# Kernel optimization log

Measured on AMD Instinct MI355X. Metric: run time of the kernel, lower is better.

The kernel has to match this reference:

```python
import jax, jax.numpy as jnp
import numpy as np

DIM = 1024
NUM_ATT = 8
NUM_HEADS = 16
HEAD_DIM = DIM // NUM_HEADS
ROPE_BASE = 10000.0
NEG_INF = -1e9


def _rope(x):
    # x: [B, H, L, hd]; torchtune-style interleaved RoPE applied along the sequence axis.
    B, H, L, hd = x.shape
    pos = jnp.arange(L, dtype=jnp.float32)
    inv_freq = 1.0 / (ROPE_BASE ** (jnp.arange(0, hd, 2, dtype=jnp.float32) / hd))
    ang = pos[:, None] * inv_freq[None, :]          # [L, hd/2]
    cos = jnp.cos(ang)[None, None]                  # [1,1,L,hd/2]
    sin = jnp.sin(ang)[None, None]
    xr = x.reshape(B, H, L, hd // 2, 2)
    x0, x1 = xr[..., 0], xr[..., 1]
    out = jnp.stack([x0 * cos - x1 * sin, x1 * cos + x0 * sin], axis=-1)
    return out.reshape(B, H, L, hd).astype(x.dtype)


def setup_inputs() -> dict:
    key = jax.random.key(0)
    ks = jax.random.split(key, 7)
    B, L = 32, 512
    x = jax.random.normal(ks[0], (B, L, DIM), dtype=jnp.float32)
    s = 0.02  # init scale for numerical sanity (init choice, not math)
    query_projs = jax.random.normal(ks[1], (NUM_ATT, DIM, DIM), dtype=jnp.float32) * s
    key_projs = jax.random.normal(ks[2], (NUM_ATT, DIM, DIM), dtype=jnp.float32) * s
    value_projs = jax.random.normal(ks[3], (NUM_ATT, DIM, DIM), dtype=jnp.float32) * s
    out_projs = jax.random.normal(ks[4], (NUM_ATT, DIM, DIM), dtype=jnp.float32) * s
    router_w = jax.random.normal(ks[5], (DIM, NUM_ATT), dtype=jnp.float32) * s
    router_b = jnp.zeros((NUM_ATT,), dtype=jnp.float32)
    return {"x": x, "query_projs": query_projs, "key_projs": key_projs,
            "value_projs": value_projs, "out_projs": out_projs,
            "router_w": router_w, "router_b": router_b}


def reference(x, query_projs, key_projs, value_projs, out_projs, router_w, router_b):
    B, L, D = x.shape
    H, hd = NUM_HEADS, HEAD_DIM
    scale = hd ** -0.5

    # top-1 routing on mean-pooled tokens
    logits = x.mean(axis=1) @ router_w + router_b       # [B, E]
    attn_probs = jax.nn.softmax(logits, axis=-1)
    routes = jnp.argmax(attn_probs, axis=-1)            # [B] int

    # per-batch weight gather (the memory-bound irregular access) + bmm
    qw = query_projs[routes]                             # [B, D, D]
    kw = key_projs[routes]
    vw = value_projs[routes]
    q = jnp.einsum('bld,bde->ble', x, qw)
    k = jnp.einsum('bld,bde->ble', x, kw)
    v = jnp.einsum('bld,bde->ble', x, vw)

    q = q.reshape(B, L, H, hd).transpose(0, 2, 1, 3)     # [B,H,L,hd]
    k = k.reshape(B, L, H, hd).transpose(0, 2, 1, 3)
    v = v.reshape(B, L, H, hd).transpose(0, 2, 1, 3)

    q = _rope(q)
    k = _rope(k)

    scores = jnp.einsum('bhld,bhmd->bhlm', q, k) * scale  # [B,H,L,L]
    causal = jnp.triu(jnp.ones((L, L), dtype=bool), k=1)  # True above diag = masked
    scores = jnp.where(causal[None, None], NEG_INF, scores)
    attn = jax.nn.softmax(scores, axis=-1)
    out = jnp.einsum('bhlm,bhmd->bhld', attn, v)          # [B,H,L,hd]
    out = out.transpose(0, 2, 1, 3).reshape(B, L, D)

    ow = out_projs[routes]                                # [B, D, D]
    out = jnp.einsum('bld,bde->ble', out, ow)
    return out, attn_probs
```

## Files before the change

### kernel.cpp

```cpp
#include <hip/hip_runtime.h>


typedef __attribute__((ext_vector_type(8))) short bf16x8;
typedef __attribute__((ext_vector_type(4))) float f32x4;
typedef __attribute__((ext_vector_type(8))) unsigned short u16x8;

typedef const __attribute__((address_space(1))) unsigned short* gas_t;
typedef __attribute__((address_space(3))) unsigned short* las_t;

#define OFF_PART   (0ull)
#define OFF_ROUTES (2ull << 20)
#define OFF_XB     (3ull << 20)
#define OFF_WT     (40ull << 20)
#define OFF_QKV    (112ull << 20)

__device__ __forceinline__ unsigned short f2bf(float f){
  unsigned int u = __float_as_uint(f);
  u += 0x7fffu + ((u >> 16) & 1u);
  return (unsigned short)(u >> 16);
}
__device__ __forceinline__ float bfu(unsigned int lo16){
  return __uint_as_float(lo16 << 16);
}


__global__ void meanpool_kernel(const float* __restrict__ x, float* __restrict__ part){
  const int b = blockIdx.x, lc = blockIdx.y, t = threadIdx.x;
  const float* xb = x + ((size_t)b*512 + lc*32)*1024;
  float a0=0.f, a1=0.f, a2=0.f, a3=0.f;
  for (int l = 0; l < 32; ++l){
    const float* row = xb + l*1024;
    a0 += row[t]; a1 += row[t+256]; a2 += row[t+512]; a3 += row[t+768];
  }
  float* o = part + ((size_t)b*16 + lc)*1024;
  o[t] = a0; o[t+256] = a1; o[t+512] = a2; o[t+768] = a3;
}

__global__ void router_kernel(const float* __restrict__ part,
                              const float* __restrict__ rw,
                              const float* __restrict__ rbias,
                              float* __restrict__ probs,
                              int* __restrict__ routes){
  const int b = blockIdx.x, t = threadIdx.x;
  __shared__ float xbar[1024];
  __shared__ float red[256*8];
  #pragma unroll
  for (int k = 0; k < 4; ++k){
    const int d = t + k*256;
    float s = 0.f;
    for (int lc = 0; lc < 16; ++lc) s += part[((size_t)b*16 + lc)*1024 + d];
    xbar[d] = s * (1.0f/512.0f);
  }
  __syncthreads();
  float p[8] = {0.f,0.f,0.f,0.f,0.f,0.f,0.f,0.f};
  #pragma unroll
  for (int k = 0; k < 4; ++k){
    const int d = t + k*256;
    const float xv = xbar[d];
    #pragma unroll
    for (int e = 0; e < 8; ++e) p[e] = fmaf(xv, rw[d*8 + e], p[e]);
  }
  #pragma unroll
  for (int e = 0; e < 8; ++e) red[t*8 + e] = p[e];
  __syncthreads();
  for (int s2 = 128; s2 > 0; s2 >>= 1){
    if (t < s2){
      #pragma unroll
      for (int e = 0; e < 8; ++e) red[t*8 + e] += red[(t + s2)*8 + e];
    }
    __syncthreads();
  }
  if (t == 0){
    float lg[8], mx = -3e38f; int am = 0;
    #pragma unroll
    for (int e = 0; e < 8; ++e){
      lg[e] = red[e] + rbias[e];
      if (lg[e] > mx){ mx = lg[e]; am = e; }
    }
    float sum = 0.f, ex[8];
    #pragma unroll
    for (int e = 0; e < 8; ++e){ ex[e] = __expf(lg[e] - mx); sum += ex[e]; }
    const float inv = 1.0f / sum;
    #pragma unroll
    for (int e = 0; e < 8; ++e) probs[b*8 + e] = ex[e] * inv;
    routes[b] = am;
  }
}


__global__ void xcast_kernel(const float4* __restrict__ x, unsigned short* __restrict__ xb){
  const size_t i = (size_t)blockIdx.x * blockDim.x + threadIdx.x;
  const float4 v = x[i];
  ushort4 o;
  o.x = f2bf(v.x); o.y = f2bf(v.y); o.z = f2bf(v.z); o.w = f2bf(v.w);
  *(ushort4*)(xb + 4*i) = o;
}

__global__ void wcast_kernel(const float* __restrict__ W, unsigned short* __restrict__ Wt){
  __shared__ float tile[32][33];
  const int mtx = blockIdx.z;
  const float* Wm = W + (size_t)mtx*1024*1024;
  unsigned short* Wo = Wt + (size_t)mtx*1024*1024;
  const int t = threadIdx.x;
  const int c = t & 31, r0 = t >> 5;
  const int gx = blockIdx.x*32, gy = blockIdx.y*32;
  #pragma unroll
  for (int k = 0; k < 4; ++k){
    const int r = r0 + k*8;
    tile[r][c] = Wm[(size_t)(gy + r)*1024 + gx + c];
  }
  __syncthreads();
  #pragma unroll
  for (int k = 0; k < 4; ++k){
    const int r = r0 + k*8;
    Wo[(size_t)(gx + r)*1024 + gy + c] = f2bf(tile[c][r]);
  }
}


template<int MODE>
__global__ __launch_bounds__(256, 2) void gemm_kernel(
    const unsigned short* __restrict__ A,
    const unsigned short* __restrict__ Wt,
    const int* __restrict__ routes,
    unsigned short* __restrict__ qkvout,
    float* __restrict__ outf)
{
  __shared__ __align__(16) unsigned short As[128*32];
  __shared__ __align__(16) unsigned short Bs[128*32];

  const int z = blockIdx.z;
  const int p = (MODE == 0) ? (z >> 5) : 0;
  const int b = (MODE == 0) ? (z & 31) : z;
  const int route = routes[b];
  const unsigned short* Ab = A + (size_t)b*512*1024;
  const unsigned short* Wb = Wt + (size_t)((MODE == 0) ? (p*8 + route) : route)*1024*1024;
  const int m0 = blockIdx.y * 128;
  const int n0 = blockIdx.x * 128;
  const int t = threadIdx.x;
  const int lane = t & 63;
  const int wave = t >> 6;
  const int wm = (wave >> 1) * 64;
  const int wn = (wave & 1) * 64;
  const int quad = lane >> 4;
  const int ln = lane & 15;

  f32x4 acc[4][4] = {};

  const int u0 = t, u1 = t + 256;
  const unsigned short* gA0 = Ab + (size_t)(m0 + (u0 >> 2))*1024 + (u0 & 3)*8;
  const unsigned short* gA1 = Ab + (size_t)(m0 + (u1 >> 2))*1024 + (u1 & 3)*8;
  const unsigned short* gB0 = Wb + (size_t)(n0 + (u0 >> 2))*1024 + (u0 & 3)*8;
  const unsigned short* gB1 = Wb + (size_t)(n0 + (u1 >> 2))*1024 + (u1 & 3)*8;
  las_t lA0 = (las_t)(As + u0*8), lA1 = (las_t)(As + u1*8);
  las_t lB0 = (las_t)(Bs + u0*8), lB1 = (las_t)(Bs + u1*8);

  const unsigned short* fa[4];
  const unsigned short* fb[4];
  #pragma unroll
  for (int i = 0; i < 4; ++i){
    fa[i] = As + (wm + i*16 + ln)*32 + quad*8;
    fb[i] = Bs + (wn + i*16 + ln)*32 + quad*8;
  }

  for (int k0 = 0; k0 < 1024; k0 += 32){
    __syncthreads();
    __builtin_amdgcn_global_load_lds((gas_t)(gA0 + k0), lA0, 16, 0, 0);
    __builtin_amdgcn_global_load_lds((gas_t)(gA1 + k0), lA1, 16, 0, 0);
    __builtin_amdgcn_global_load_lds((gas_t)(gB0 + k0), lB0, 16, 0, 0);
    __builtin_amdgcn_global_load_lds((gas_t)(gB1 + k0), lB1, 16, 0, 0);
    __syncthreads();
    bf16x8 av[4], bv[4];
    #pragma unroll
    for (int i = 0; i < 4; ++i){
      av[i] = *(const bf16x8*)fa[i];
      bv[i] = *(const bf16x8*)fb[i];
    }
    #pragma unroll
    for (int i = 0; i < 4; ++i)
      #pragma unroll
      for (int j = 0; j < 4; ++j)
        acc[i][j] = __builtin_amdgcn_mfma_f32_16x16x32_bf16(av[i], bv[j], acc[i][j], 0, 0, 0);
  }

  if (MODE == 0){
    const bool dorope = (p < 2);
    #pragma unroll
    for (int j = 0; j < 4; ++j){
      const int e  = n0 + wn + j*16 + ln;
      const int h  = e >> 6;
      const int eh = e & 63;
      const float invf = exp2f(-0.41524101f * (float)(eh >> 1));
      unsigned short* outp = qkvout + ((((size_t)p*32 + b)*16 + h)*512)*64 + eh;
      #pragma unroll
      for (int i = 0; i < 4; ++i){
        #pragma unroll
        for (int r = 0; r < 4; ++r){
          const int l = m0 + wm + i*16 + quad*4 + r;
          const float own = acc[i][j][r];
          float v = own;
          if (dorope){
            const float par = __shfl_xor(own, 1, 64);
            float sn, cs;
            __sincosf((float)l * invf, &sn, &cs);
            v = (e & 1) ? fmaf(own, cs, par*sn) : fmaf(own, cs, -par*sn);
          }
          outp[(size_t)l*64] = f2bf(v);
        }
      }
    }
  } else {
    #pragma unroll
    for (int j = 0; j < 4; ++j){
      const int e = n0 + wn + j*16 + ln;
      #pragma unroll
      for (int i = 0; i < 4; ++i){
        #pragma unroll
        for (int r = 0; r < 4; ++r){
          const int l = m0 + wm + i*16 + quad*4 + r;
          outf[((size_t)b*512 + l)*1024 + e] = acc[i][j][r];
        }
      }
    }
  }
}


#define PSTR 72

__global__ __launch_bounds__(256, 2) void attn_kernel(
    const unsigned short* __restrict__ qkv,
    unsigned short* __restrict__ ctx)
{
  __shared__ __align__(16) unsigned short Qs[64*64];
  __shared__ __align__(16) unsigned short Ks[64*64];
  __shared__ __align__(16) unsigned short Vt[64*64];
  __shared__ __align__(16) unsigned short Ps[64*PSTR];

  const int qt = blockIdx.x, h = blockIdx.y, b = blockIdx.z;
  const size_t HO  = (((size_t)b)*16 + h)*512*64;
  const size_t PSZ = (size_t)32*16*512*64;
  const unsigned short* Qg = qkv + HO + (size_t)qt*4096;
  const unsigned short* Kg = qkv + PSZ + HO;
  const unsigned short* Vg = qkv + 2*PSZ + HO;

  const int t    = threadIdx.x;
  const int lane = t & 63;
  const int wave = t >> 6;
  const int quad = lane >> 4;
  const int ln   = lane & 15;
  const int wq   = wave * 16;

  __builtin_amdgcn_global_load_lds((gas_t)(Qg + t*8),       (las_t)(Qs + t*8),       16, 0, 0);
  __builtin_amdgcn_global_load_lds((gas_t)(Qg + (t+256)*8), (las_t)(Qs + (t+256)*8), 16, 0, 0);

  const int va = t & 31;
  const int vg = t >> 5;
  unsigned int* Vt32 = (unsigned int*)Vt;

  float m_r[4], l_r[4];
  #pragma unroll
  for (int r = 0; r < 4; ++r){ m_r[r] = -3e38f; l_r[r] = 0.f; }
  f32x4 o[4] = {};

  const unsigned short* aQ = Qs + (wq + ln)*64 + quad*8;
  const unsigned short* bK = Ks + ln*64 + quad*8;
  const unsigned short* aP = Ps + (wq + ln)*PSTR + quad*8;
  const unsigned short* bV = Vt + ln*64 + quad*8;

  for (int kt = 0; kt <= qt; ++kt){
    __syncthreads();
    const unsigned short* Ktile = Kg + kt*4096;
    __builtin_amdgcn_global_load_lds((gas_t)(Ktile + t*8),       (las_t)(Ks + t*8),       16, 0, 0);
    __builtin_amdgcn_global_load_lds((gas_t)(Ktile + (t+256)*8), (las_t)(Ks + (t+256)*8), 16, 0, 0);
    {
      const unsigned short* vb = Vg + kt*4096 + (2*va)*64 + vg*8;
      const u16x8 r0 = *(const u16x8*)vb;
      const u16x8 r1 = *(const u16x8*)(vb + 64);
      #pragma unroll
      for (int i = 0; i < 8; ++i)
        Vt32[(vg*8 + i)*32 + va] = (unsigned int)r0[i] | ((unsigned int)r1[i] << 16);
    }
    __syncthreads();

    f32x4 s[4] = {};
    #pragma unroll
    for (int ks = 0; ks < 2; ++ks){
      const bf16x8 aq = *(const bf16x8*)(aQ + ks*32);
      #pragma unroll
      for (int kn = 0; kn < 4; ++kn){
        const bf16x8 bk = *(const bf16x8*)(bK + kn*1024 + ks*32);
        s[kn] = __builtin_amdgcn_mfma_f32_16x16x32_bf16(aq, bk, s[kn], 0, 0, 0);
      }
    }

    const bool diag = (kt == qt);
    float p[4][4], lm[4];
    #pragma unroll
    for (int r = 0; r < 4; ++r) lm[r] = -3e38f;
    #pragma unroll
    for (int kn = 0; kn < 4; ++kn){
      const int col = kn*16 + ln;
      #pragma unroll
      for (int r = 0; r < 4; ++r){
        float v = s[kn][r] * 0.125f;
        if (diag && col > wq + quad*4 + r) v = -1e9f;
        p[kn][r] = v;
        lm[r] = fmaxf(lm[r], v);
      }
    }
    #pragma unroll
    for (int off = 1; off < 16; off <<= 1)
      #pragma unroll
      for (int r = 0; r < 4; ++r)
        lm[r] = fmaxf(lm[r], __shfl_xor(lm[r], off, 64));
    float alpha[4], rsum[4];
    #pragma unroll
    for (int r = 0; r < 4; ++r){
      const float mn = fmaxf(m_r[r], lm[r]);
      alpha[r] = __expf(m_r[r] - mn);
      m_r[r] = mn;
    }
    #pragma unroll
    for (int kn = 0; kn < 4; ++kn)
      #pragma unroll
      for (int r = 0; r < 4; ++r)
        p[kn][r] = __expf(p[kn][r] - m_r[r]);
    #pragma unroll
    for (int r = 0; r < 4; ++r)
      rsum[r] = (p[0][r] + p[1][r]) + (p[2][r] + p[3][r]);
    #pragma unroll
    for (int off = 1; off < 16; off <<= 1)
      #pragma unroll
      for (int r = 0; r < 4; ++r)
        rsum[r] += __shfl_xor(rsum[r], off, 64);
    #pragma unroll
    for (int r = 0; r < 4; ++r) l_r[r] = l_r[r]*alpha[r] + rsum[r];
    #pragma unroll
    for (int dn = 0; dn < 4; ++dn)
      #pragma unroll
      for (int r = 0; r < 4; ++r)
        o[dn][r] *= alpha[r];

    #pragma unroll
    for (int kn = 0; kn < 4; ++kn)
      #pragma unroll
      for (int r = 0; r < 4; ++r)
        Ps[(wq + quad*4 + r)*PSTR + kn*16 + ln] = f2bf(p[kn][r]);

    #pragma unroll
    for (int ks = 0; ks < 2; ++ks){
      const bf16x8 ap = *(const bf16x8*)(aP + ks*32);
      #pragma unroll
      for (int dn = 0; dn < 4; ++dn){
        const bf16x8 bv = *(const bf16x8*)(bV + dn*1024 + ks*32);
        o[dn] = __builtin_amdgcn_mfma_f32_16x16x32_bf16(ap, bv, o[dn], 0, 0, 0);
      }
    }
  }

  #pragma unroll
  for (int r = 0; r < 4; ++r){
    const float inv = 1.0f / l_r[r];
    unsigned short* op = ctx + ((size_t)b*512 + qt*64 + wq + quad*4 + r)*1024 + h*64 + ln;
    #pragma unroll
    for (int dn = 0; dn < 4; ++dn)
      op[dn*16] = f2bf(o[dn][r] * inv);
  }
}


extern "C" void kernel_launch(void* const* d_in, const int* in_sizes, int n_in,
                              void* d_out, int out_size, void* d_ws, size_t ws_size,
                              hipStream_t stream) {
  const float* x     = (const float*)d_in[0];
  const float* qw    = (const float*)d_in[1];
  const float* kw    = (const float*)d_in[2];
  const float* vw    = (const float*)d_in[3];
  const float* ow    = (const float*)d_in[4];
  const float* rw    = (const float*)d_in[5];
  const float* rbias = (const float*)d_in[6];
  float* out = (float*)d_out;
  char* ws = (char*)d_ws;

  float* part            = (float*)(ws + OFF_PART);
  int* routes            = (int*)(ws + OFF_ROUTES);
  unsigned short* xb     = (unsigned short*)(ws + OFF_XB);
  unsigned short* wt     = (unsigned short*)(ws + OFF_WT);
  unsigned short* qkvbuf = (unsigned short*)(ws + OFF_QKV);
  unsigned short* ctx    = xb;
  float* probs = out + (size_t)32*512*1024;

  meanpool_kernel<<<dim3(32, 16), 256, 0, stream>>>(x, part);
  router_kernel<<<32, 256, 0, stream>>>(part, rw, rbias, probs, routes);
  xcast_kernel<<<16384, 256, 0, stream>>>((const float4*)x, xb);
  wcast_kernel<<<dim3(32, 32, 8), 256, 0, stream>>>(qw, wt);
  wcast_kernel<<<dim3(32, 32, 8), 256, 0, stream>>>(kw, wt + (size_t)8*1024*1024);
  wcast_kernel<<<dim3(32, 32, 8), 256, 0, stream>>>(vw, wt + (size_t)16*1024*1024);
  wcast_kernel<<<dim3(32, 32, 8), 256, 0, stream>>>(ow, wt + (size_t)24*1024*1024);
  gemm_kernel<0><<<dim3(8, 4, 96), 256, 0, stream>>>(xb, wt, routes, qkvbuf, nullptr);
  attn_kernel<<<dim3(8, 16, 32), 256, 0, stream>>>(qkvbuf, ctx);
  gemm_kernel<1><<<dim3(8, 4, 32), 256, 0, stream>>>(ctx, wt + (size_t)24*1024*1024, routes,
                                                     nullptr, out);
}
```

Before: 616.9 us.

## Fuse x cast into meanpool, swizzle GEMM LDS, restructure attention with double-buffered K/V

Folds the fp32-to-bf16 cast of x into the mean-pool kernel so x is read once. Adds an XOR swizzle to the GEMM LDS layout to reduce bank conflicts. The QKV GEMM now writes V pre-transposed so attention no longer transposes it per tile. Attention is rewritten to handle 128 query rows per block with Q held in registers, double-buffered K/V tiles fetched asynchronously into swizzled LDS, per-wave P buffers, and a higher occupancy hint. This adds register pressure and changes the tile ordering.

Result: faster. 560.8 us (-9.1%).

```diff
diff --git a/kernel.cpp b/kernel.cpp
--- a/kernel.cpp
+++ b/kernel.cpp
@@ -3,7 +3,6 @@
 
 typedef __attribute__((ext_vector_type(8))) short bf16x8;
 typedef __attribute__((ext_vector_type(4))) float f32x4;
-typedef __attribute__((ext_vector_type(8))) unsigned short u16x8;
 
 typedef const __attribute__((address_space(1))) unsigned short* gas_t;
 typedef __attribute__((address_space(3))) unsigned short* las_t;
@@ -19,18 +18,21 @@
   u += 0x7fffu + ((u >> 16) & 1u);
   return (unsigned short)(u >> 16);
 }
-__device__ __forceinline__ float bfu(unsigned int lo16){
-  return __uint_as_float(lo16 << 16);
-}
-
-
-__global__ void meanpool_kernel(const float* __restrict__ x, float* __restrict__ part){
+
+
+__global__ void meanpool_kernel(const float* __restrict__ x, float* __restrict__ part,
+                                unsigned short* __restrict__ xb){
   const int b = blockIdx.x, lc = blockIdx.y, t = threadIdx.x;
-  const float* xb = x + ((size_t)b*512 + lc*32)*1024;
+  const size_t base = ((size_t)b*512 + lc*32)*1024;
+  const float* xs = x + base;
+  unsigned short* xo = xb + base;
   float a0=0.f, a1=0.f, a2=0.f, a3=0.f;
   for (int l = 0; l < 32; ++l){
-    const float* row = xb + l*1024;
-    a0 += row[t]; a1 += row[t+256]; a2 += row[t+512]; a3 += row[t+768];
+    const float* row = xs + l*1024;
+    unsigned short* orow = xo + l*1024;
+    const float v0 = row[t], v1 = row[t+256], v2 = row[t+512], v3 = row[t+768];
+    a0 += v0; a1 += v1; a2 += v2; a3 += v3;
+    orow[t] = f2bf(v0); orow[t+256] = f2bf(v1); orow[t+512] = f2bf(v2); orow[t+768] = f2bf(v3);
   }
   float* o = part + ((size_t)b*16 + lc)*1024;
   o[t] = a0; o[t+256] = a1; o[t+512] = a2; o[t+768] = a3;
@@ -87,14 +89,6 @@
   }
 }
 
-
-__global__ void xcast_kernel(const float4* __restrict__ x, unsigned short* __restrict__ xb){
-  const size_t i = (size_t)blockIdx.x * blockDim.x + threadIdx.x;
-  const float4 v = x[i];
-  ushort4 o;
-  o.x = f2bf(v.x); o.y = f2bf(v.y); o.z = f2bf(v.z); o.w = f2bf(v.w);
-  *(ushort4*)(xb + 4*i) = o;
-}
 
 __global__ void wcast_kernel(const float* __restrict__ W, unsigned short* __restrict__ Wt){
   __shared__ float tile[32][33];
@@ -148,19 +142,22 @@
   f32x4 acc[4][4] = {};
 
   const int u0 = t, u1 = t + 256;
-  const unsigned short* gA0 = Ab + (size_t)(m0 + (u0 >> 2))*1024 + (u0 & 3)*8;
-  const unsigned short* gA1 = Ab + (size_t)(m0 + (u1 >> 2))*1024 + (u1 & 3)*8;
-  const unsigned short* gB0 = Wb + (size_t)(n0 + (u0 >> 2))*1024 + (u0 & 3)*8;
-  const unsigned short* gB1 = Wb + (size_t)(n0 + (u1 >> 2))*1024 + (u1 & 3)*8;
+  const int r0s = u0 >> 2, c0s = (u0 & 3) ^ ((r0s >> 1) & 3);
+  const int r1s = u1 >> 2, c1s = (u1 & 3) ^ ((r1s >> 1) & 3);
+  const unsigned short* gA0 = Ab + (size_t)(m0 + r0s)*1024 + c0s*8;
+  const unsigned short* gA1 = Ab + (size_t)(m0 + r1s)*1024 + c1s*8;
+  const unsigned short* gB0 = Wb + (size_t)(n0 + r0s)*1024 + c0s*8;
+  const unsigned short* gB1 = Wb + (size_t)(n0 + r1s)*1024 + c1s*8;
   las_t lA0 = (las_t)(As + u0*8), lA1 = (las_t)(As + u1*8);
   las_t lB0 = (las_t)(Bs + u0*8), lB1 = (las_t)(Bs + u1*8);
 
+  const int swz = (quad ^ ((ln >> 1) & 3)) * 8;
   const unsigned short* fa[4];
   const unsigned short* fb[4];
   #pragma unroll
   for (int i = 0; i < 4; ++i){
-    fa[i] = As + (wm + i*16 + ln)*32 + quad*8;
-    fb[i] = Bs + (wn + i*16 + ln)*32 + quad*8;
+    fa[i] = As + (wm + i*16 + ln)*32 + swz;
+    fb[i] = Bs + (wn + i*16 + ln)*32 + swz;
   }
 
   for (int k0 = 0; k0 < 1024; k0 += 32){
@@ -184,28 +181,43 @@
   }
 
   if (MODE == 0){
-    const bool dorope = (p < 2);
-    #pragma unroll
-    for (int j = 0; j < 4; ++j){
-      const int e  = n0 + wn + j*16 + ln;
-      const int h  = e >> 6;
-      const int eh = e & 63;
-      const float invf = exp2f(-0.41524101f * (float)(eh >> 1));
-      unsigned short* outp = qkvout + ((((size_t)p*32 + b)*16 + h)*512)*64 + eh;
-      #pragma unroll
-      for (int i = 0; i < 4; ++i){
-        #pragma unroll
-        for (int r = 0; r < 4; ++r){
-          const int l = m0 + wm + i*16 + quad*4 + r;
-          const float own = acc[i][j][r];
-          float v = own;
-          if (dorope){
+    const size_t PSZ = (size_t)32*16*512*64;
+    if (p < 2){
+      #pragma unroll
+      for (int j = 0; j < 4; ++j){
+        const int e  = n0 + wn + j*16 + ln;
+        const int h  = e >> 6;
+        const int eh = e & 63;
+        const float invf = exp2f(-0.41524101f * (float)(eh >> 1));
+        unsigned short* outp = qkvout + ((((size_t)p*32 + b)*16 + h)*512)*64 + eh;
+        #pragma unroll
+        for (int i = 0; i < 4; ++i){
+          #pragma unroll
+          for (int r = 0; r < 4; ++r){
+            const int l = m0 + wm + i*16 + quad*4 + r;
+            const float own = acc[i][j][r];
             const float par = __shfl_xor(own, 1, 64);
             float sn, cs;
             __sincosf((float)l * invf, &sn, &cs);
-            v = (e & 1) ? fmaf(own, cs, par*sn) : fmaf(own, cs, -par*sn);
+            const float v = (e & 1) ? fmaf(own, cs, par*sn) : fmaf(own, cs, -par*sn);
+            outp[(size_t)l*64] = f2bf(v);
           }
-          outp[(size_t)l*64] = f2bf(v);
+        }
+      }
+    } else {
+      #pragma unroll
+      for (int j = 0; j < 4; ++j){
+        const int e  = n0 + wn + j*16 + ln;
+        const int h  = e >> 6;
+        const int eh = e & 63;
+        unsigned short* outp = qkvout + 2*PSZ + (((size_t)b*16 + h)*64 + eh)*512;
+        #pragma unroll
+        for (int i = 0; i < 4; ++i){
+          const int l0 = m0 + wm + i*16 + quad*4;
+          ushort4 pk;
+          pk.x = f2bf(acc[i][j][0]); pk.y = f2bf(acc[i][j][1]);
+          pk.z = f2bf(acc[i][j][2]); pk.w = f2bf(acc[i][j][3]);
+          *(ushort4*)(outp + l0) = pk;
         }
       }
     }
@@ -228,144 +240,162 @@
 
 #define PSTR 72
 
-__global__ __launch_bounds__(256, 2) void attn_kernel(
+__global__ __launch_bounds__(256, 3) void attn_kernel(
     const unsigned short* __restrict__ qkv,
     unsigned short* __restrict__ ctx)
 {
-  __shared__ __align__(16) unsigned short Qs[64*64];
-  __shared__ __align__(16) unsigned short Ks[64*64];
-  __shared__ __align__(16) unsigned short Vt[64*64];
-  __shared__ __align__(16) unsigned short Ps[64*PSTR];
+  __shared__ __align__(16) unsigned short Ks[2][64*64];
+  __shared__ __align__(16) unsigned short Vts[2][64*64];
+  __shared__ __align__(16) unsigned short Ps[4][32*PSTR];
 
   const int qt = blockIdx.x, h = blockIdx.y, b = blockIdx.z;
   const size_t HO  = (((size_t)b)*16 + h)*512*64;
   const size_t PSZ = (size_t)32*16*512*64;
-  const unsigned short* Qg = qkv + HO + (size_t)qt*4096;
-  const unsigned short* Kg = qkv + PSZ + HO;
-  const unsigned short* Vg = qkv + 2*PSZ + HO;
+  const unsigned short* Qg  = qkv + HO;
+  const unsigned short* Kg  = qkv + PSZ + HO;
+  const unsigned short* Vtg = qkv + 2*PSZ + HO;
 
   const int t    = threadIdx.x;
   const int lane = t & 63;
   const int wave = t >> 6;
   const int quad = lane >> 4;
   const int ln   = lane & 15;
-  const int wq   = wave * 16;
-
-  __builtin_amdgcn_global_load_lds((gas_t)(Qg + t*8),       (las_t)(Qs + t*8),       16, 0, 0);
-  __builtin_amdgcn_global_load_lds((gas_t)(Qg + (t+256)*8), (las_t)(Qs + (t+256)*8), 16, 0, 0);
-
-  const int va = t & 31;
-  const int vg = t >> 5;
-  unsigned int* Vt32 = (unsigned int*)Vt;
-
-  float m_r[4], l_r[4];
-  #pragma unroll
-  for (int r = 0; r < 4; ++r){ m_r[r] = -3e38f; l_r[r] = 0.f; }
-  f32x4 o[4] = {};
-
-  const unsigned short* aQ = Qs + (wq + ln)*64 + quad*8;
-  const unsigned short* bK = Ks + ln*64 + quad*8;
-  const unsigned short* aP = Ps + (wq + ln)*PSTR + quad*8;
-  const unsigned short* bV = Vt + ln*64 + quad*8;
-
-  for (int kt = 0; kt <= qt; ++kt){
+
+  const int u0 = t, u1 = t + 256;
+  const int kr0 = u0 >> 3, kc0 = (u0 & 7) ^ (kr0 & 7);
+  const int kr1 = u1 >> 3, kc1 = (u1 & 7) ^ (kr1 & 7);
+
+  bf16x8 aq[2][2];
+  #pragma unroll
+  for (int rg = 0; rg < 2; ++rg){
+    const int row = qt*128 + rg*64 + wave*16 + ln;
+    #pragma unroll
+    for (int ks = 0; ks < 2; ++ks)
+      aq[rg][ks] = *(const bf16x8*)(Qg + (size_t)row*64 + ks*32 + quad*8);
+  }
+
+  const int ktEnd = 2*qt + 1;
+
+  __builtin_amdgcn_global_load_lds((gas_t)(Kg  + kr0*64  + kc0*8), (las_t)(Ks[0]  + u0*8), 16,0,0);
+  __builtin_amdgcn_global_load_lds((gas_t)(Kg  + kr1*64  + kc1*8), (las_t)(Ks[0]  + u1*8), 16,0,0);
+  __builtin_amdgcn_global_load_lds((gas_t)(Vtg + kr0*512 + kc0*8), (las_t)(Vts[0] + u0*8), 16,0,0);
+  __builtin_amdgcn_global_load_lds((gas_t)(Vtg + kr1*512 + kc1*8), (las_t)(Vts[0] + u1*8), 16,0,0);
+
+  float m_r[2][4], l_r[2][4];
+  #pragma unroll
+  for (int rg = 0; rg < 2; ++rg)
+    #pragma unroll
+    for (int r = 0; r < 4; ++r){ m_r[rg][r] = -3e38f; l_r[rg][r] = 0.f; }
+  f32x4 o[2][4] = {};
+
+  const int swzl = ln & 7;
+  unsigned short* Pw = Ps[wave];
+  const int rowoff = wave*16 + quad*4;
+
+  for (int kt = 0; kt <= ktEnd; ++kt){
     __syncthreads();
-    const unsigned short* Ktile = Kg + kt*4096;
-    __builtin_amdgcn_global_load_lds((gas_t)(Ktile + t*8),       (las_t)(Ks + t*8),       16, 0, 0);
-    __builtin_amdgcn_global_load_lds((gas_t)(Ktile + (t+256)*8), (las_t)(Ks + (t+256)*8), 16, 0, 0);
-    {
-      const unsigned short* vb = Vg + kt*4096 + (2*va)*64 + vg*8;
-      const u16x8 r0 = *(const u16x8*)vb;
-      const u16x8 r1 = *(const u16x8*)(vb + 64);
-      #pragma unroll
-      for (int i = 0; i < 8; ++i)
-        Vt32[(vg*8 + i)*32 + va] = (unsigned int)r0[i] | ((unsigned int)r1[i] << 16);
-    }
-    __syncthreads();
-
-    f32x4 s[4] = {};
-    #pragma unroll
-    for (int ks = 0; ks < 2; ++ks){
-      const bf16x8 aq = *(const bf16x8*)(aQ + ks*32);
+    if (kt < ktEnd){
+      const unsigned short* Kn  = Kg + (kt+1)*4096;
+      const int col = (kt+1)*64;
+      unsigned short* kb = Ks[(kt+1)&1];
+      unsigned short* vb = Vts[(kt+1)&1];
+      __builtin_amdgcn_global_load_lds((gas_t)(Kn  + kr0*64 + kc0*8),        (las_t)(kb + u0*8), 16,0,0);
+      __builtin_amdgcn_global_load_lds((gas_t)(Kn  + kr1*64 + kc1*8),        (las_t)(kb + u1*8), 16,0,0);
+      __builtin_amdgcn_global_load_lds((gas_t)(Vtg + kr0*512 + col + kc0*8), (las_t)(vb + u0*8), 16,0,0);
+      __builtin_amdgcn_global_load_lds((gas_t)(Vtg + kr1*512 + col + kc1*8), (las_t)(vb + u1*8), 16,0,0);
+    }
+    const unsigned short* ks_ = Ks[kt&1];
+    const unsigned short* vt_ = Vts[kt&1];
+
+    #pragma unroll
+    for (int rg = 0; rg < 2; ++rg){
+      if (rg == 0 && kt > 2*qt) continue;
+      const bool diag = (kt == 2*qt + rg);
+
+      f32x4 s[4] = {};
+      #pragma unroll
+      for (int ks2 = 0; ks2 < 2; ++ks2){
+        #pragma unroll
+        for (int kn = 0; kn < 4; ++kn){
+          const bf16x8 bk = *(const bf16x8*)(ks_ + (kn*16+ln)*64 + (((quad + ks2*4) ^ swzl))*8);
+          s[kn] = __builtin_amdgcn_mfma_f32_16x16x32_bf16(aq[rg][ks2], bk, s[kn], 0, 0, 0);
+        }
+      }
+
+      float p[4][4], lm[4] = {-3e38f,-3e38f,-3e38f,-3e38f};
       #pragma unroll
       for (int kn = 0; kn < 4; ++kn){
-        const bf16x8 bk = *(const bf16x8*)(bK + kn*1024 + ks*32);
-        s[kn] = __builtin_amdgcn_mfma_f32_16x16x32_bf16(aq, bk, s[kn], 0, 0, 0);
-      }
-    }
-
-    const bool diag = (kt == qt);
-    float p[4][4], lm[4];
-    #pragma unroll
-    for (int r = 0; r < 4; ++r) lm[r] = -3e38f;
-    #pragma unroll
-    for (int kn = 0; kn < 4; ++kn){
-      const int col = kn*16 + ln;
+        const int col = kn*16 + ln;
+        #pragma unroll
+        for (int r = 0; r < 4; ++r){
+          float v = s[kn][r] * 0.125f;
+          if (diag && col > rowoff + r) v = -1e9f;
+          p[kn][r] = v;
+          lm[r] = fmaxf(lm[r], v);
+        }
+      }
+      #pragma unroll
+      for (int off = 1; off < 16; off <<= 1)
+        #pragma unroll
+        for (int r = 0; r < 4; ++r)
+          lm[r] = fmaxf(lm[r], __shfl_xor(lm[r], off, 64));
+      float alpha[4], rsum[4];
       #pragma unroll
       for (int r = 0; r < 4; ++r){
-        float v = s[kn][r] * 0.125f;
-        if (diag && col > wq + quad*4 + r) v = -1e9f;
-        p[kn][r] = v;
-        lm[r] = fmaxf(lm[r], v);
-      }
-    }
-    #pragma unroll
-    for (int off = 1; off < 16; off <<= 1)
+        const float mn = fmaxf(m_r[rg][r], lm[r]);
+        alpha[r] = __expf(m_r[rg][r] - mn);
+        m_r[rg][r] = mn;
+      }
+      #pragma unroll
+      for (int kn = 0; kn < 4; ++kn)
+        #pragma unroll
+        for (int r = 0; r < 4; ++r)
+          p[kn][r] = __expf(p[kn][r] - m_r[rg][r]);
       #pragma unroll
       for (int r = 0; r < 4; ++r)
-        lm[r] = fmaxf(lm[r], __shfl_xor(lm[r], off, 64));
-    float alpha[4], rsum[4];
+        rsum[r] = (p[0][r] + p[1][r]) + (p[2][r] + p[3][r]);
+      #pragma unroll
+      for (int off = 1; off < 16; off <<= 1)
+        #pragma unroll
+        for (int r = 0; r < 4; ++r)
+          rsum[r] += __shfl_xor(rsum[r], off, 64);
+      #pragma unroll
+      for (int r = 0; r < 4; ++r) l_r[rg][r] = l_r[rg][r]*alpha[r] + rsum[r];
+      #pragma unroll
+      for (int dn = 0; dn < 4; ++dn)
+        #pragma unroll
+        for (int r = 0; r < 4; ++r)
+          o[rg][dn][r] *= alpha[r];
+
+      #pragma unroll
+      for (int kn = 0; kn < 4; ++kn)
+        #pragma unroll
+        for (int r = 0; r < 4; ++r)
+          Pw[(rg*16 + quad*4 + r)*PSTR + kn*16 + ln] = f2bf(p[kn][r]);
+
+      #pragma unroll
+      for (int ks2 = 0; ks2 < 2; ++ks2){
+        const bf16x8 ap = *(const bf16x8*)(Pw + (rg*16 + ln)*PSTR + quad*8 + ks2*32);
+        #pragma unroll
+        for (int dn = 0; dn < 4; ++dn){
+          const bf16x8 bv = *(const bf16x8*)(vt_ + (dn*16+ln)*64 + (((quad + ks2*4) ^ swzl))*8);
+          o[rg][dn] = __builtin_amdgcn_mfma_f32_16x16x32_bf16(ap, bv, o[rg][dn], 0, 0, 0);
+        }
+      }
+    }
+  }
+
+  #pragma unroll
+  for (int rg = 0; rg < 2; ++rg){
     #pragma unroll
     for (int r = 0; r < 4; ++r){
-      const float mn = fmaxf(m_r[r], lm[r]);
-      alpha[r] = __expf(m_r[r] - mn);
-      m_r[r] = mn;
-    }
-    #pragma unroll
-    for (int kn = 0; kn < 4; ++kn)
-      #pragma unroll
-      for (int r = 0; r < 4; ++r)
-        p[kn][r] = __expf(p[kn][r] - m_r[r]);
-    #pragma unroll
-    for (int r = 0; r < 4; ++r)
-      rsum[r] = (p[0][r] + p[1][r]) + (p[2][r] + p[3][r]);
-    #pragma unroll
-    for (int off = 1; off < 16; off <<= 1)
-      #pragma unroll
-      for (int r = 0; r < 4; ++r)
-        rsum[r] += __shfl_xor(rsum[r], off, 64);
-    #pragma unroll
-    for (int r = 0; r < 4; ++r) l_r[r] = l_r[r]*alpha[r] + rsum[r];
-    #pragma unroll
-    for (int dn = 0; dn < 4; ++dn)
-      #pragma unroll
-      for (int r = 0; r < 4; ++r)
-        o[dn][r] *= alpha[r];
-
-    #pragma unroll
-    for (int kn = 0; kn < 4; ++kn)
-      #pragma unroll
-      for (int r = 0; r < 4; ++r)
-        Ps[(wq + quad*4 + r)*PSTR + kn*16 + ln] = f2bf(p[kn][r]);
-
-    #pragma unroll
-    for (int ks = 0; ks < 2; ++ks){
-      const bf16x8 ap = *(const bf16x8*)(aP + ks*32);
-      #pragma unroll
-      for (int dn = 0; dn < 4; ++dn){
-        const bf16x8 bv = *(const bf16x8*)(bV + dn*1024 + ks*32);
-        o[dn] = __builtin_amdgcn_mfma_f32_16x16x32_bf16(ap, bv, o[dn], 0, 0, 0);
-      }
-    }
-  }
-
-  #pragma unroll
-  for (int r = 0; r < 4; ++r){
-    const float inv = 1.0f / l_r[r];
-    unsigned short* op = ctx + ((size_t)b*512 + qt*64 + wq + quad*4 + r)*1024 + h*64 + ln;
-    #pragma unroll
-    for (int dn = 0; dn < 4; ++dn)
-      op[dn*16] = f2bf(o[dn][r] * inv);
+      const float inv = 1.0f / l_r[rg][r];
+      const int row = qt*128 + rg*64 + wave*16 + quad*4 + r;
+      unsigned short* op = ctx + ((size_t)b*512 + row)*1024 + h*64 + ln;
+      #pragma unroll
+      for (int dn = 0; dn < 4; ++dn)
+        op[dn*16] = f2bf(o[rg][dn][r] * inv);
+    }
   }
 }
 
@@ -391,15 +421,14 @@
   unsigned short* ctx    = xb;
   float* probs = out + (size_t)32*512*1024;
 
-  meanpool_kernel<<<dim3(32, 16), 256, 0, stream>>>(x, part);
+  meanpool_kernel<<<dim3(32, 16), 256, 0, stream>>>(x, part, xb);
   router_kernel<<<32, 256, 0, stream>>>(part, rw, rbias, probs, routes);
-  xcast_kernel<<<16384, 256, 0, stream>>>((const float4*)x, xb);
   wcast_kernel<<<dim3(32, 32, 8), 256, 0, stream>>>(qw, wt);
   wcast_kernel<<<dim3(32, 32, 8), 256, 0, stream>>>(kw, wt + (size_t)8*1024*1024);
   wcast_kernel<<<dim3(32, 32, 8), 256, 0, stream>>>(vw, wt + (size_t)16*1024*1024);
   wcast_kernel<<<dim3(32, 32, 8), 256, 0, stream>>>(ow, wt + (size_t)24*1024*1024);
   gemm_kernel<0><<<dim3(8, 4, 96), 256, 0, stream>>>(xb, wt, routes, qkvbuf, nullptr);
-  attn_kernel<<<dim3(8, 16, 32), 256, 0, stream>>>(qkvbuf, ctx);
+  attn_kernel<<<dim3(4, 16, 32), 256, 0, stream>>>(qkvbuf, ctx);
   gemm_kernel<1><<<dim3(8, 4, 32), 256, 0, stream>>>(ctx, wt + (size_t)24*1024*1024, routes,
                                                      nullptr, out);
 }
```
